# Kernel optimization log

Measured on AMD Instinct MI355X. Metric: run time of the kernel, lower is better.

Reference implementation:

```python
import jax, jax.numpy as jnp
import numpy as np

B, L, D = 16, 512, 768   # batch, seq_len, hidden_size
H = 12                   # encoder attention heads (self_attention_scores)
K = 128                  # num_preserved_tokens
U, NH = 256, 4           # router attention num_units / num_heads


def setup_inputs() -> dict:
    key = jax.random.key(0)
    ks = jax.random.split(key, 8)
    hidden_states = jax.random.normal(ks[0], (B, L, D), dtype=jnp.float32)
    u = jax.random.uniform(ks[1], (B, 1, 1, L))
    attention_mask = jnp.where(u < 0.9, 0.0, -10000.0).astype(jnp.float32)
    self_attention_scores = jax.random.normal(ks[2], (B, H, L, L), dtype=jnp.float32)
    Wq = jax.random.normal(ks[3], (U, D), dtype=jnp.float32) * 0.02
    Wk = jax.random.normal(ks[4], (U, D), dtype=jnp.float32) * 0.02
    Wv = jax.random.normal(ks[5], (U, D), dtype=jnp.float32) * 0.02
    Wo = jax.random.normal(ks[6], (D, U), dtype=jnp.float32) * 0.02
    bo = jnp.zeros((D,), dtype=jnp.float32)
    return {"hidden_states": hidden_states, "attention_mask": attention_mask,
            "self_attention_scores": self_attention_scores,
            "Wq": Wq, "Wk": Wk, "Wv": Wv, "Wo": Wo, "bo": bo}


def reference(hidden_states, attention_mask, self_attention_scores, Wq, Wk, Wv, Wo, bo):
    # sentence summary: softmax over additive mask -> weighted token average
    att = jax.nn.softmax(attention_mask, axis=-1)            # [B,1,1,L]
    sentences = jnp.einsum('bql,bld->bqd', att[:, 0], hidden_states)  # [B,1,D]

    key_padding_mask = attention_mask[:, 0, 0, :] < -10.0    # [B,L] True = masked

    # MyMultiHeadAttention(query=sentences, key=value=hidden_states)
    hd = U // NH
    q = jnp.einsum('bqd,ud->bqu', sentences, Wq)             # [B,1,U]
    k = jnp.einsum('bld,ud->blu', hidden_states, Wk)         # [B,L,U]
    v = jnp.einsum('bld,ud->blu', hidden_states, Wv)         # [B,L,U]
    qh = q.reshape(B, 1, NH, hd).transpose(2, 0, 1, 3)       # [h,B,1,hd]
    kh = k.reshape(B, L, NH, hd).transpose(2, 0, 1, 3)       # [h,B,L,hd]
    vh = v.reshape(B, L, NH, hd).transpose(2, 0, 1, 3)       # [h,B,L,hd]
    # NOTE: original scales by key_dim**0.5 = hidden_size**0.5 (not head dim)
    scores = jnp.einsum('hbqd,hbkd->hbqk', qh, kh) / (D ** 0.5)  # [h,B,1,L]
    scores = jnp.where(key_padding_mask[None, :, None, :], -jnp.inf, scores)
    probs = jax.nn.softmax(scores, axis=-1)
    out_h = jnp.einsum('hbqk,hbkd->hbqd', probs, vh)         # [h,B,1,hd]
    out = out_h.transpose(1, 2, 0, 3).reshape(B, 1, U)       # concat heads
    new_token = jnp.einsum('bqu,du->bqd', out, Wo) + bo      # [B,1,D]

    class_token = hidden_states[:, :1, :]                    # [B,1,D]

    # importance: mean over heads, sum over query positions -> [B,L]
    importance = self_attention_scores.mean(axis=1).sum(axis=1)
    top_idx = jax.lax.top_k(importance, K)[1]                # [B,K]
    # boolean-mask gather preserves original token order -> sort indices
    sorted_idx = jnp.sort(top_idx, axis=-1)                  # [B,K]
    preserved_tokens = jnp.take_along_axis(hidden_states, sorted_idx[:, :, None], axis=1)  # [B,K,D]
    preserved_mask = jnp.take_along_axis(attention_mask[:, 0, 0, :], sorted_idx, axis=1)
    preserved_mask = preserved_mask.reshape(B, 1, 1, K)

    zmask = jnp.zeros((B, 1, 1, 1), dtype=attention_mask.dtype)
    final_token = jnp.concatenate([class_token, preserved_tokens, new_token], axis=1)  # [B,K+2,D]
    final_attention_mask = jnp.concatenate([zmask, preserved_mask, zmask], axis=-1)    # [B,1,1,K+2]
    return final_token, final_attention_mask
```

## Files before the change

### kernel.cpp

```cpp
#include <hip/hip_runtime.h>
#include <math.h>

#define B_ 16
#define L_ 512
#define D_ 768
#define H_ 12
#define K_ 128
#define U_ 256
#define NH_ 4
#define HD_ 64
#define OUTROWS_ 130
#define IMP_G_ 96

__device__ __forceinline__ float blk_max768(float v, float* red, int t) {
  __syncthreads();
  #pragma unroll
  for (int o = 32; o > 0; o >>= 1) v = fmaxf(v, __shfl_down(v, o, 64));
  if ((t & 63) == 0) red[t >> 6] = v;
  __syncthreads();
  if (t == 0) {
    float r = red[0];
    #pragma unroll
    for (int w = 1; w < 12; ++w) r = fmaxf(r, red[w]);
    red[0] = r;
  }
  __syncthreads();
  return red[0];
}

__device__ __forceinline__ float blk_sum768(float v, float* red, int t) {
  __syncthreads();
  #pragma unroll
  for (int o = 32; o > 0; o >>= 1) v += __shfl_down(v, o, 64);
  if ((t & 63) == 0) red[t >> 6] = v;
  __syncthreads();
  if (t == 0) {
    float r = 0.f;
    #pragma unroll
    for (int w = 0; w < 12; ++w) r += red[w];
    red[0] = r;
  }
  __syncthreads();
  return red[0];
}

__global__ __launch_bounds__(256) void importance_kernel(
    const float* __restrict__ scores, float* __restrict__ part) {
  const int b = blockIdx.y, chunk = blockIdx.x, t = threadIdx.x;
  const int qcol = t & 127;
  const int rhalf = t >> 7;
  const float4* base = (const float4*)scores +
      ((size_t)(b * (H_ * L_) + chunk * 128 + rhalf)) * 128 + qcol;
  float4 a = make_float4(0.f, 0.f, 0.f, 0.f);
  #pragma unroll 8
  for (int r = 0; r < 64; ++r) {
    float4 v = base[(size_t)r * 256];
    a.x += v.x; a.y += v.y; a.z += v.z; a.w += v.w;
  }
  const float s = 1.0f / 12.0f;
  float4 o = make_float4(a.x * s, a.y * s, a.z * s, a.w * s);
  ((float4*)part)[((size_t)b * IMP_G_ + chunk * 2 + rhalf) * 128 + qcol] = o;
}

__global__ __launch_bounds__(768) void sent_kernel(
    const float* __restrict__ hidden, const float* __restrict__ mask,
    float* __restrict__ sent_part) {
  __shared__ float att[L_];
  __shared__ float red[16];
  const int b = blockIdx.x, chunk = blockIdx.y, t = threadIdx.x;
  float m = (t < L_) ? mask[b * L_ + t] : -INFINITY;
  float mx = blk_max768(m, red, t);
  float e = (t < L_) ? expf(m - mx) : 0.f;
  float se = blk_sum768(e, red, t);
  if (t < L_) att[t] = e / se;
  __syncthreads();
  const int l0 = chunk * 32;
  const float* hp = hidden + ((size_t)b * L_ + l0) * D_ + t;
  float acc = 0.f;
  #pragma unroll 8
  for (int l = 0; l < 32; ++l) acc += att[l0 + l] * hp[(size_t)l * D_];
  sent_part[((size_t)b * 16 + chunk) * D_ + t] = acc;
}

__global__ __launch_bounds__(768) void qproj_topk_kernel(
    const float* __restrict__ sent_part, const float* __restrict__ Wq,
    const float* __restrict__ Wk, float* __restrict__ wqe,
    const float* __restrict__ part, const float* __restrict__ mask,
    const float* __restrict__ hidden, float* __restrict__ out0,
    float* __restrict__ out1) {
  __shared__ float s[D_];
  __shared__ float qvh[HD_];
  __shared__ float v[L_];
  __shared__ int lidx[K_];
  __shared__ int wcnt[12];
  const int t = threadIdx.x;
  const int wave = t >> 6, lane = t & 63;

  if (blockIdx.x < 64) {
    const int b = blockIdx.x >> 2, h = blockIdx.x & 3;
    {
      const float* sp = sent_part + (size_t)b * 16 * D_ + t;
      float a = 0.f;
      #pragma unroll
      for (int c = 0; c < 16; ++c) a += sp[(size_t)c * D_];
      s[t] = a;
    }
    __syncthreads();
    for (int u = wave; u < HD_; u += 12) {
      const float* wr = Wq + (size_t)(h * HD_ + u) * D_;
      float acc = 0.f;
      #pragma unroll
      for (int k = 0; k < 12; ++k) {
        const int d = lane + (k << 6);
        acc += wr[d] * s[d];
      }
      #pragma unroll
      for (int o = 32; o > 0; o >>= 1) acc += __shfl_down(acc, o, 64);
      if (lane == 0) qvh[u] = acc;
    }
    __syncthreads();
    {
      float acc = 0.f;
      const float* wk = Wk + (size_t)(h * HD_) * D_ + t;
      #pragma unroll 4
      for (int j = 0; j < HD_; ++j) acc += qvh[j] * wk[(size_t)j * D_];
      wqe[((size_t)b * NH_ + h) * D_ + t] = acc;
    }
  } else {
    const int b = blockIdx.x - 64;
    if (t < L_) {
      const float* pp = part + (size_t)b * IMP_G_ * L_ + t;
      float sum = 0.f;
      #pragma unroll 8
      for (int g = 0; g < IMP_G_; ++g) sum += pp[(size_t)g * L_];
      v[t] = sum;
    }
    __syncthreads();
    bool sel = false;
    if (t < L_) {
      const float mv = v[t];
      int cnt = 0;
      #pragma unroll 8
      for (int j = 0; j < L_; ++j) {
        float o = v[j];
        cnt += (o > mv) || (o == mv && j < t);
      }
      sel = cnt < K_;
    }
    const unsigned long long ball = __ballot(sel);
    if (lane == 0) wcnt[wave] = __popcll(ball);
    __syncthreads();
    int base = 0;
    for (int w = 0; w < wave; ++w) base += wcnt[w];
    const int pos = base + __popcll(ball & ((1ull << lane) - 1ull));
    if (sel) {
      lidx[pos] = t;
      out1[b * OUTROWS_ + 1 + pos] = mask[b * L_ + t];
    }
    if (t == 0) {
      out1[b * OUTROWS_ + 0] = 0.f;
      out1[b * OUTROWS_ + OUTROWS_ - 1] = 0.f;
    }
    __syncthreads();
    const float4* hb4 = (const float4*)(hidden + (size_t)b * L_ * D_);
    float4* ob4 = (float4*)(out0 + (size_t)b * OUTROWS_ * D_);
    const int NG = (K_ + 1) * 192;
    for (int i = t; i < NG; i += 768) {
      const int r = i / 192;
      const int c = i - r * 192;
      const int src = (r == 0) ? 0 : lidx[r - 1];
      ob4[r * 192 + c] = hb4[src * 192 + c];
    }
  }
}

__global__ __launch_bounds__(256) void score_kernel(
    const float* __restrict__ hidden, const float* __restrict__ mask,
    const float* __restrict__ wqe, float* __restrict__ scores) {
  __shared__ float4 wq4[NH_ * 192];
  const int b = blockIdx.x, chunk = blockIdx.y, t = threadIdx.x;
  {
    const float4* wsrc = (const float4*)(wqe + (size_t)b * NH_ * D_);
    for (int i = t; i < NH_ * 192; i += 256) wq4[i] = wsrc[i];
  }
  __syncthreads();
  const int wave = t >> 6, lane = t & 63;
  const float scale = 0.03608439182435161f;
  #pragma unroll
  for (int r = 0; r < 8; ++r) {
    const int l = chunk * 32 + wave * 8 + r;
    const float4* hr4 = (const float4*)(hidden + ((size_t)b * L_ + l) * D_);
    float s0 = 0.f, s1 = 0.f, s2 = 0.f, s3 = 0.f;
    #pragma unroll
    for (int jj = 0; jj < 3; ++jj) {
      const int c = lane + 64 * jj;
      const float4 hv = hr4[c];
      const float4 w0 = wq4[0 * 192 + c];
      const float4 w1 = wq4[1 * 192 + c];
      const float4 w2 = wq4[2 * 192 + c];
      const float4 w3 = wq4[3 * 192 + c];
      s0 += hv.x * w0.x + hv.y * w0.y + hv.z * w0.z + hv.w * w0.w;
      s1 += hv.x * w1.x + hv.y * w1.y + hv.z * w1.z + hv.w * w1.w;
      s2 += hv.x * w2.x + hv.y * w2.y + hv.z * w2.z + hv.w * w2.w;
      s3 += hv.x * w3.x + hv.y * w3.y + hv.z * w3.z + hv.w * w3.w;
    }
    #pragma unroll
    for (int o = 32; o > 0; o >>= 1) {
      s0 += __shfl_down(s0, o, 64);
      s1 += __shfl_down(s1, o, 64);
      s2 += __shfl_down(s2, o, 64);
      s3 += __shfl_down(s3, o, 64);
    }
    if (lane == 0) {
      const bool kp = mask[b * L_ + l] < -10.f;
      float* sp = scores + (size_t)b * NH_ * L_ + l;
      sp[0 * L_] = kp ? -INFINITY : s0 * scale;
      sp[1 * L_] = kp ? -INFINITY : s1 * scale;
      sp[2 * L_] = kp ? -INFINITY : s2 * scale;
      sp[3 * L_] = kp ? -INFINITY : s3 * scale;
    }
  }
}

__global__ __launch_bounds__(768) void ctx_prob_kernel(
    const float* __restrict__ hidden, const float* __restrict__ scores,
    float* __restrict__ ctx_part) {
  __shared__ float pr[NH_][32];
  __shared__ float red[16];
  const int b = blockIdx.x, chunk = blockIdx.y, t = threadIdx.x;
  const int l0 = chunk * 32;
  #pragma unroll
  for (int h = 0; h < NH_; ++h) {
    const float* sp = scores + ((size_t)b * NH_ + h) * L_;
    float val = (t < L_) ? sp[t] : -INFINITY;
    float mx = blk_max768(val, red, t);
    float e = (t < L_) ? expf(val - mx) : 0.f;
    float se = blk_sum768(e, red, t);
    if (t >= l0 && t < l0 + 32) pr[h][t - l0] = e / se;
  }
  __syncthreads();
  const float* hp = hidden + ((size_t)b * L_ + l0) * D_ + t;
  float c0 = 0.f, c1 = 0.f, c2 = 0.f, c3 = 0.f;
  #pragma unroll 8
  for (int l = 0; l < 32; ++l) {
    float hv = hp[(size_t)l * D_];
    c0 += pr[0][l] * hv;
    c1 += pr[1][l] * hv;
    c2 += pr[2][l] * hv;
    c3 += pr[3][l] * hv;
  }
  float* cb = ctx_part + ((size_t)b * 16 + chunk) * NH_ * D_ + t;
  cb[0 * D_] = c0;
  cb[1 * D_] = c1;
  cb[2 * D_] = c2;
  cb[3 * D_] = c3;
}

__global__ __launch_bounds__(768) void outv_kernel(
    const float* __restrict__ ctx_part, const float* __restrict__ Wv,
    float* __restrict__ outv) {
  __shared__ float ch[D_];
  const int b = blockIdx.x, h = blockIdx.y, t = threadIdx.x;
  const int wave = t >> 6, lane = t & 63;
  {
    float a = 0.f;
    #pragma unroll
    for (int c = 0; c < 16; ++c)
      a += ctx_part[(((size_t)b * 16 + c) * NH_ + h) * D_ + t];
    ch[t] = a;
  }
  __syncthreads();
  for (int u = wave; u < HD_; u += 12) {
    const float* wr = Wv + (size_t)(h * HD_ + u) * D_;
    float acc = 0.f;
    #pragma unroll
    for (int k = 0; k < 12; ++k) {
      const int d = lane + (k << 6);
      acc += wr[d] * ch[d];
    }
    #pragma unroll
    for (int o = 32; o > 0; o >>= 1) acc += __shfl_down(acc, o, 64);
    if (lane == 0) outv[b * U_ + h * HD_ + u] = acc;
  }
}

__global__ __launch_bounds__(192) void newtoken_kernel(
    const float* __restrict__ outv, const float* __restrict__ Wo,
    const float* __restrict__ bo, float* __restrict__ out0) {
  __shared__ float4 ov4[64];
  const int b = blockIdx.x, q = blockIdx.y, t = threadIdx.x;
  const int wave = t >> 6, lane = t & 63;
  if (t < 64) ov4[t] = ((const float4*)(outv + b * U_))[t];
  __syncthreads();
  const int dbase = q * 192 + wave * 64;
  const float4 o = ov4[lane];
  for (int i = 0; i < 64; ++i) {
    const int d = dbase + i;
    const float4 w = ((const float4*)(Wo + (size_t)d * U_))[lane];
    float acc = w.x * o.x + w.y * o.y + w.z * o.z + w.w * o.w;
    #pragma unroll
    for (int off = 32; off > 0; off >>= 1) acc += __shfl_down(acc, off, 64);
    if (lane == 0)
      out0[((size_t)b * OUTROWS_ + (OUTROWS_ - 1)) * D_ + d] = bo[d] + acc;
  }
}

extern "C" void kernel_launch(void* const* d_in, const int* in_sizes, int n_in,
                              void* d_out, int out_size, void* d_ws, size_t ws_size,
                              hipStream_t stream) {
  const float* hidden = (const float*)d_in[0];
  const float* mask   = (const float*)d_in[1];
  const float* sas    = (const float*)d_in[2];
  const float* Wq     = (const float*)d_in[3];
  const float* Wk     = (const float*)d_in[4];
  const float* Wv     = (const float*)d_in[5];
  const float* Wo     = (const float*)d_in[6];
  const float* bo     = (const float*)d_in[7];

  float* out0 = (float*)d_out;
  float* out1 = out0 + (size_t)B_ * OUTROWS_ * D_;

  float* part      = (float*)d_ws;
  float* sent_part = part + (size_t)B_ * IMP_G_ * L_;
  float* ctx_part  = sent_part + (size_t)B_ * 16 * D_;
  float* wqe       = ctx_part + (size_t)B_ * 16 * NH_ * D_;
  float* scores    = wqe + (size_t)B_ * NH_ * D_;
  float* outv      = scores + (size_t)B_ * NH_ * L_;

  importance_kernel<<<dim3(48, B_), 256, 0, stream>>>(sas, part);
  sent_kernel<<<dim3(B_, 16), 768, 0, stream>>>(hidden, mask, sent_part);
  qproj_topk_kernel<<<80, 768, 0, stream>>>(sent_part, Wq, Wk, wqe,
                                            part, mask, hidden, out0, out1);
  score_kernel<<<dim3(B_, 16), 256, 0, stream>>>(hidden, mask, wqe, scores);
  ctx_prob_kernel<<<dim3(B_, 16), 768, 0, stream>>>(hidden, scores, ctx_part);
  outv_kernel<<<dim3(B_, NH_), 768, 0, stream>>>(ctx_part, Wv, outv);
  newtoken_kernel<<<dim3(B_, 4), 192, 0, stream>>>(outv, Wo, bo, out0);
}
```

Baseline: 401.4 us.

## Merge importance and sentence kernels; fuse ctx with Wv projection via atomics

The importance reduction and the sentence-summary pass now run in one launch, and each importance block now covers more rows (96 rows per block, 64 chunks) with an LDS reduction. The ctx and outv kernels are fused so each chunk block projects its partial context through Wv and atomically adds into outv, which is zeroed earlier in the topk blocks. Softmax reductions use fewer barriers, and the hidden-state reads now use float4. This removes two launches and the ctx_part round trip, but each of the 256 blocks reads all of Wv and outv now relies on float atomics, which are not order-deterministic.

```diff
diff --git a/kernel.cpp b/kernel.cpp
--- a/kernel.cpp
+++ b/kernel.cpp
@@ -10,76 +10,88 @@
 #define NH_ 4
 #define HD_ 64
 #define OUTROWS_ 130
-#define IMP_G_ 96
-
-__device__ __forceinline__ float blk_max768(float v, float* red, int t) {
-  __syncthreads();
-  #pragma unroll
-  for (int o = 32; o > 0; o >>= 1) v = fmaxf(v, __shfl_down(v, o, 64));
-  if ((t & 63) == 0) red[t >> 6] = v;
-  __syncthreads();
-  if (t == 0) {
-    float r = red[0];
-    #pragma unroll
-    for (int w = 1; w < 12; ++w) r = fmaxf(r, red[w]);
-    red[0] = r;
-  }
-  __syncthreads();
-  return red[0];
-}
-
-__device__ __forceinline__ float blk_sum768(float v, float* red, int t) {
-  __syncthreads();
-  #pragma unroll
-  for (int o = 32; o > 0; o >>= 1) v += __shfl_down(v, o, 64);
-  if ((t & 63) == 0) red[t >> 6] = v;
-  __syncthreads();
-  if (t == 0) {
-    float r = 0.f;
-    #pragma unroll
-    for (int w = 0; w < 12; ++w) r += red[w];
-    red[0] = r;
-  }
-  __syncthreads();
-  return red[0];
-}
-
-__global__ __launch_bounds__(256) void importance_kernel(
-    const float* __restrict__ scores, float* __restrict__ part) {
-  const int b = blockIdx.y, chunk = blockIdx.x, t = threadIdx.x;
-  const int qcol = t & 127;
-  const int rhalf = t >> 7;
-  const float4* base = (const float4*)scores +
-      ((size_t)(b * (H_ * L_) + chunk * 128 + rhalf)) * 128 + qcol;
-  float4 a = make_float4(0.f, 0.f, 0.f, 0.f);
-  #pragma unroll 8
-  for (int r = 0; r < 64; ++r) {
-    float4 v = base[(size_t)r * 256];
-    a.x += v.x; a.y += v.y; a.z += v.z; a.w += v.w;
-  }
-  const float s = 1.0f / 12.0f;
-  float4 o = make_float4(a.x * s, a.y * s, a.z * s, a.w * s);
-  ((float4*)part)[((size_t)b * IMP_G_ + chunk * 2 + rhalf) * 128 + qcol] = o;
-}
-
-__global__ __launch_bounds__(768) void sent_kernel(
-    const float* __restrict__ hidden, const float* __restrict__ mask,
+#define IMPCH_ 64
+
+__global__ __launch_bounds__(768) void front_kernel(
+    const float* __restrict__ sas, const float* __restrict__ hidden,
+    const float* __restrict__ mask, float* __restrict__ part,
     float* __restrict__ sent_part) {
-  __shared__ float att[L_];
-  __shared__ float red[16];
-  const int b = blockIdx.x, chunk = blockIdx.y, t = threadIdx.x;
-  float m = (t < L_) ? mask[b * L_ + t] : -INFINITY;
-  float mx = blk_max768(m, red, t);
-  float e = (t < L_) ? expf(m - mx) : 0.f;
-  float se = blk_sum768(e, red, t);
-  if (t < L_) att[t] = e / se;
-  __syncthreads();
-  const int l0 = chunk * 32;
-  const float* hp = hidden + ((size_t)b * L_ + l0) * D_ + t;
-  float acc = 0.f;
-  #pragma unroll 8
-  for (int l = 0; l < 32; ++l) acc += att[l0 + l] * hp[(size_t)l * D_];
-  sent_part[((size_t)b * 16 + chunk) * D_ + t] = acc;
+  const int t = threadIdx.x;
+  if (blockIdx.x < B_ * IMPCH_) {
+    __shared__ float4 lbuf[6][128];
+    const int b = blockIdx.x >> 6, chunk = blockIdx.x & 63;
+    const int col4 = t & 127;
+    const int rg = t >> 7;
+    const float4* base = (const float4*)sas +
+        ((size_t)(b * (H_ * L_) + chunk * 96 + rg * 16)) * 128 + col4;
+    float4 a = make_float4(0.f, 0.f, 0.f, 0.f);
+    #pragma unroll
+    for (int k = 0; k < 16; ++k) {
+      float4 v = base[(size_t)k * 128];
+      a.x += v.x; a.y += v.y; a.z += v.z; a.w += v.w;
+    }
+    lbuf[rg][col4] = a;
+    __syncthreads();
+    if (rg == 0) {
+      float4 o = lbuf[0][col4];
+      #pragma unroll
+      for (int g = 1; g < 6; ++g) {
+        float4 v = lbuf[g][col4];
+        o.x += v.x; o.y += v.y; o.z += v.z; o.w += v.w;
+      }
+      const float s = 1.0f / 12.0f;
+      o.x *= s; o.y *= s; o.z *= s; o.w *= s;
+      ((float4*)part)[((size_t)b * IMPCH_ + chunk) * 128 + col4] = o;
+    }
+  } else {
+    __shared__ float att[L_];
+    __shared__ float red_m[12], red_s[12];
+    __shared__ float4 cbuf[4][192];
+    const int i = blockIdx.x - B_ * IMPCH_;
+    const int b = i >> 4, chunk = i & 15;
+    const int wave = t >> 6, lane = t & 63;
+    const float m = (t < L_) ? mask[b * L_ + t] : -INFINITY;
+    float r = m;
+    #pragma unroll
+    for (int off = 32; off > 0; off >>= 1) r = fmaxf(r, __shfl_down(r, off, 64));
+    if (lane == 0) red_m[wave] = r;
+    __syncthreads();
+    float mx = red_m[0];
+    #pragma unroll
+    for (int w = 1; w < 12; ++w) mx = fmaxf(mx, red_m[w]);
+    const float e = (t < L_) ? expf(m - mx) : 0.f;
+    float rs = e;
+    #pragma unroll
+    for (int off = 32; off > 0; off >>= 1) rs += __shfl_down(rs, off, 64);
+    if (lane == 0) red_s[wave] = rs;
+    __syncthreads();
+    float se = 0.f;
+    #pragma unroll
+    for (int w = 0; w < 12; ++w) se += red_s[w];
+    if (t < L_) att[t] = e / se;
+    __syncthreads();
+    const int c4 = t % 192, sub = t / 192;
+    const int l0 = chunk * 32 + sub * 8;
+    const float4* h4 = (const float4*)hidden + ((size_t)b * L_ + l0) * 192 + c4;
+    float4 acc = make_float4(0.f, 0.f, 0.f, 0.f);
+    #pragma unroll
+    for (int ii = 0; ii < 8; ++ii) {
+      const float w = att[l0 + ii];
+      const float4 hv = h4[(size_t)ii * 192];
+      acc.x += w * hv.x; acc.y += w * hv.y; acc.z += w * hv.z; acc.w += w * hv.w;
+    }
+    cbuf[sub][c4] = acc;
+    __syncthreads();
+    if (t < 192) {
+      float4 o = cbuf[0][t];
+      #pragma unroll
+      for (int g = 1; g < 4; ++g) {
+        const float4 v = cbuf[g][t];
+        o.x += v.x; o.y += v.y; o.z += v.z; o.w += v.w;
+      }
+      ((float4*)sent_part)[((size_t)b * 16 + chunk) * 192 + t] = o;
+    }
+  }
 }
 
 __global__ __launch_bounds__(768) void qproj_topk_kernel(
@@ -87,7 +99,7 @@
     const float* __restrict__ Wk, float* __restrict__ wqe,
     const float* __restrict__ part, const float* __restrict__ mask,
     const float* __restrict__ hidden, float* __restrict__ out0,
-    float* __restrict__ out1) {
+    float* __restrict__ out1, float* __restrict__ outv) {
   __shared__ float s[D_];
   __shared__ float qvh[HD_];
   __shared__ float v[L_];
@@ -128,11 +140,12 @@
     }
   } else {
     const int b = blockIdx.x - 64;
+    if (t < U_) outv[b * U_ + t] = 0.f;
     if (t < L_) {
-      const float* pp = part + (size_t)b * IMP_G_ * L_ + t;
+      const float* pp = part + (size_t)b * IMPCH_ * L_ + t;
       float sum = 0.f;
       #pragma unroll 8
-      for (int g = 0; g < IMP_G_; ++g) sum += pp[(size_t)g * L_];
+      for (int g = 0; g < IMPCH_; ++g) sum += pp[(size_t)g * L_];
       v[t] = sum;
     }
     __syncthreads();
@@ -222,65 +235,76 @@
   }
 }
 
-__global__ __launch_bounds__(768) void ctx_prob_kernel(
+__global__ __launch_bounds__(768) void ctx_outv_kernel(
     const float* __restrict__ hidden, const float* __restrict__ scores,
-    float* __restrict__ ctx_part) {
+    const float* __restrict__ Wv, float* __restrict__ outv) {
   __shared__ float pr[NH_][32];
-  __shared__ float red[16];
+  __shared__ float red_m[NH_][12], red_s[NH_][12];
+  __shared__ __align__(16) float ctxs[NH_ * D_];
   const int b = blockIdx.x, chunk = blockIdx.y, t = threadIdx.x;
+  const int wave = t >> 6, lane = t & 63;
   const int l0 = chunk * 32;
+
+  float val[NH_];
+  #pragma unroll
+  for (int h = 0; h < NH_; ++h)
+    val[h] = (t < L_) ? scores[((size_t)b * NH_ + h) * L_ + t] : -INFINITY;
   #pragma unroll
   for (int h = 0; h < NH_; ++h) {
-    const float* sp = scores + ((size_t)b * NH_ + h) * L_;
-    float val = (t < L_) ? sp[t] : -INFINITY;
-    float mx = blk_max768(val, red, t);
-    float e = (t < L_) ? expf(val - mx) : 0.f;
-    float se = blk_sum768(e, red, t);
-    if (t >= l0 && t < l0 + 32) pr[h][t - l0] = e / se;
-  }
-  __syncthreads();
-  const float* hp = hidden + ((size_t)b * L_ + l0) * D_ + t;
-  float c0 = 0.f, c1 = 0.f, c2 = 0.f, c3 = 0.f;
+    float r = val[h];
+    #pragma unroll
+    for (int off = 32; off > 0; off >>= 1) r = fmaxf(r, __shfl_down(r, off, 64));
+    if (lane == 0) red_m[h][wave] = r;
+  }
+  __syncthreads();
+  float e[NH_];
+  #pragma unroll
+  for (int h = 0; h < NH_; ++h) {
+    float mx = red_m[h][0];
+    #pragma unroll
+    for (int w = 1; w < 12; ++w) mx = fmaxf(mx, red_m[h][w]);
+    e[h] = (t < L_) ? expf(val[h] - mx) : 0.f;
+    float rs = e[h];
+    #pragma unroll
+    for (int off = 32; off > 0; off >>= 1) rs += __shfl_down(rs, off, 64);
+    if (lane == 0) red_s[h][wave] = rs;
+  }
+  __syncthreads();
+  if (t >= l0 && t < l0 + 32) {
+    #pragma unroll
+    for (int h = 0; h < NH_; ++h) {
+      float se = 0.f;
+      #pragma unroll
+      for (int w = 0; w < 12; ++w) se += red_s[h][w];
+      pr[h][t - l0] = e[h] / se;
+    }
+  }
+  __syncthreads();
+
+  const int c4 = t % 192, hh = t / 192;
+  const float4* h4 = (const float4*)hidden + ((size_t)b * L_ + l0) * 192 + c4;
+  float4 acc = make_float4(0.f, 0.f, 0.f, 0.f);
   #pragma unroll 8
   for (int l = 0; l < 32; ++l) {
-    float hv = hp[(size_t)l * D_];
-    c0 += pr[0][l] * hv;
-    c1 += pr[1][l] * hv;
-    c2 += pr[2][l] * hv;
-    c3 += pr[3][l] * hv;
-  }
-  float* cb = ctx_part + ((size_t)b * 16 + chunk) * NH_ * D_ + t;
-  cb[0 * D_] = c0;
-  cb[1 * D_] = c1;
-  cb[2 * D_] = c2;
-  cb[3 * D_] = c3;
-}
-
-__global__ __launch_bounds__(768) void outv_kernel(
-    const float* __restrict__ ctx_part, const float* __restrict__ Wv,
-    float* __restrict__ outv) {
-  __shared__ float ch[D_];
-  const int b = blockIdx.x, h = blockIdx.y, t = threadIdx.x;
-  const int wave = t >> 6, lane = t & 63;
-  {
+    const float w = pr[hh][l];
+    const float4 hv = h4[(size_t)l * 192];
+    acc.x += w * hv.x; acc.y += w * hv.y; acc.z += w * hv.z; acc.w += w * hv.w;
+  }
+  ((float4*)ctxs)[hh * 192 + c4] = acc;
+  __syncthreads();
+
+  for (int hu = wave; hu < U_; hu += 12) {
+    const float* wr = Wv + (size_t)hu * D_;
+    const float* ch = ctxs + (hu >> 6) * D_;
     float a = 0.f;
-    #pragma unroll
-    for (int c = 0; c < 16; ++c)
-      a += ctx_part[(((size_t)b * 16 + c) * NH_ + h) * D_ + t];
-    ch[t] = a;
-  }
-  __syncthreads();
-  for (int u = wave; u < HD_; u += 12) {
-    const float* wr = Wv + (size_t)(h * HD_ + u) * D_;
-    float acc = 0.f;
     #pragma unroll
     for (int k = 0; k < 12; ++k) {
       const int d = lane + (k << 6);
-      acc += wr[d] * ch[d];
-    }
-    #pragma unroll
-    for (int o = 32; o > 0; o >>= 1) acc += __shfl_down(acc, o, 64);
-    if (lane == 0) outv[b * U_ + h * HD_ + u] = acc;
+      a += wr[d] * ch[d];
+    }
+    #pragma unroll
+    for (int off = 32; off > 0; off >>= 1) a += __shfl_down(a, off, 64);
+    if (lane == 0) atomicAdd(&outv[b * U_ + hu], a);
   }
 }
 
@@ -321,18 +345,16 @@
   float* out1 = out0 + (size_t)B_ * OUTROWS_ * D_;
 
   float* part      = (float*)d_ws;
-  float* sent_part = part + (size_t)B_ * IMP_G_ * L_;
-  float* ctx_part  = sent_part + (size_t)B_ * 16 * D_;
-  float* wqe       = ctx_part + (size_t)B_ * 16 * NH_ * D_;
+  float* sent_part = part + (size_t)B_ * IMPCH_ * L_;
+  float* wqe       = sent_part + (size_t)B_ * 16 * D_;
   float* scores    = wqe + (size_t)B_ * NH_ * D_;
   float* outv      = scores + (size_t)B_ * NH_ * L_;
 
-  importance_kernel<<<dim3(48, B_), 256, 0, stream>>>(sas, part);
-  sent_kernel<<<dim3(B_, 16), 768, 0, stream>>>(hidden, mask, sent_part);
+  front_kernel<<<B_ * IMPCH_ + B_ * 16, 768, 0, stream>>>(sas, hidden, mask,
+                                                          part, sent_part);
   qproj_topk_kernel<<<80, 768, 0, stream>>>(sent_part, Wq, Wk, wqe,
-                                            part, mask, hidden, out0, out1);
+                                            part, mask, hidden, out0, out1, outv);
   score_kernel<<<dim3(B_, 16), 256, 0, stream>>>(hidden, mask, wqe, scores);
-  ctx_prob_kernel<<<dim3(B_, 16), 768, 0, stream>>>(hidden, scores, ctx_part);
-  outv_kernel<<<dim3(B_, NH_), 768, 0, stream>>>(ctx_part, Wv, outv);
+  ctx_outv_kernel<<<dim3(B_, 16), 768, 0, stream>>>(hidden, scores, Wv, outv);
   newtoken_kernel<<<dim3(B_, 4), 192, 0, stream>>>(outv, Wo, bo, out0);
 }
```

New measurement: 413.2 us. 2.9% more time.
